# Performance work log

Measured on AMD Instinct MI355X. Metric: run time of the kernel, lower is better.

Reference implementation:

```python
import jax, jax.numpy as jnp
import numpy as np

B, S, E = 8, 1024, 1024
MS = 128            # modal_context seq len
NH = 16             # attention heads
NE = 8              # total experts (4 shared + 4 modality-specific)
TOP_K = 2
FF = 4 * E          # expert hidden dim
EPS = 1e-5


def layer_norm(x, w, b, eps=EPS):
    m = jnp.mean(x, axis=-1, keepdims=True)
    v = jnp.mean(jnp.square(x - m), axis=-1, keepdims=True)
    return (x - m) / jnp.sqrt(v + eps) * w + b


def mha(q_in, kv_in, in_w, in_b, out_w, out_b, nh=NH):
    # torch nn.MultiheadAttention (batch_first) equivalent, eval mode (no dropout)
    e = q_in.shape[-1]
    q = q_in @ in_w[:e].T + in_b[:e]
    k = kv_in @ in_w[e:2 * e].T + in_b[e:2 * e]
    v = kv_in @ in_w[2 * e:].T + in_b[2 * e:]
    b, sq, _ = q.shape
    sk = k.shape[1]
    hd = e // nh
    q = q.reshape(b, sq, nh, hd).transpose(0, 2, 1, 3)
    k = k.reshape(b, sk, nh, hd).transpose(0, 2, 1, 3)
    v = v.reshape(b, sk, nh, hd).transpose(0, 2, 1, 3)
    scores = jnp.einsum('bhqd,bhkd->bhqk', q, k) * (1.0 / np.sqrt(hd).astype(np.float32))
    attn = jax.nn.softmax(scores, axis=-1)
    o = jnp.einsum('bhqk,bhkd->bhqd', attn, v).transpose(0, 2, 1, 3).reshape(b, sq, e)
    return o @ out_w.T + out_b


def _forward(x, modal_context,
             attn_in_w, attn_in_b, attn_out_w, attn_out_b,
             xattn_in_w, xattn_in_b, xattn_out_w, xattn_out_b,
             norm1_w, norm1_b, norm2_w, norm2_b, norm3_w, norm3_b,
             xnorm_w, xnorm_b, router_w, router_b, gate_w, gate_b,
             exp_ln_w, exp_ln_b, exp_fc1_w, exp_fc1_b, exp_fc2_w, exp_fc2_b):
    # --- self-attention block (pre-norm residual) ---
    h = x + mha(layer_norm(x, norm1_w, norm1_b), layer_norm(x, norm1_w, norm1_b),
                attn_in_w, attn_in_b, attn_out_w, attn_out_b)
    # --- cross-modal fusion with sigmoid modal gate ---
    xn = layer_norm(h, xnorm_w, xnorm_b)
    fusion = mha(xn, modal_context, xattn_in_w, xattn_in_b, xattn_out_w, xattn_out_b)
    gate = jax.nn.sigmoid(xn @ gate_w.T + gate_b)
    h = h + gate * fusion
    # --- MoE block: AttentiveRouter (softmax + top-k renorm) over shared+modality experts ---
    xn2 = layer_norm(h, norm2_w, norm2_b)
    logits = xn2 @ router_w.T + router_b                  # [B,S,NE]
    probs = jax.nn.softmax(logits, axis=-1)
    topw, topi = jax.lax.top_k(probs, TOP_K)              # [B,S,K]
    topw = topw / jnp.sum(topw, axis=-1, keepdims=True)
    # scatter top-k weights to dense combine tensor [B,S,NE]
    combine = jnp.sum(jax.nn.one_hot(topi, NE, dtype=x.dtype) * topw[..., None], axis=-2)
    moe = jnp.zeros_like(h)
    for e_idx in range(NE):  # small fixed loop over experts
        xe = layer_norm(xn2, exp_ln_w[e_idx], exp_ln_b[e_idx])
        hh = jax.nn.gelu(xe @ exp_fc1_w[e_idx].T + exp_fc1_b[e_idx])
        oe = hh @ exp_fc2_w[e_idx].T + exp_fc2_b[e_idx]
        moe = moe + combine[..., e_idx:e_idx + 1] * oe
    out = h + moe
    return layer_norm(out, norm3_w, norm3_b)


def setup_inputs() -> dict:
    key = jax.random.key(0)
    ks = jax.random.split(key, 32)
    std = 0.02
    d = {
        'x': jax.random.normal(ks[0], (B, S, E), jnp.float32),
        'modal_context': jax.random.normal(ks[1], (B, MS, E), jnp.float32),
        'attn_in_w': jax.random.normal(ks[2], (3 * E, E), jnp.float32) * std,
        'attn_in_b': jnp.zeros((3 * E,), jnp.float32),
        'attn_out_w': jax.random.normal(ks[3], (E, E), jnp.float32) * std,
        'attn_out_b': jnp.zeros((E,), jnp.float32),
        'xattn_in_w': jax.random.normal(ks[4], (3 * E, E), jnp.float32) * std,
        'xattn_in_b': jnp.zeros((3 * E,), jnp.float32),
        'xattn_out_w': jax.random.normal(ks[5], (E, E), jnp.float32) * std,
        'xattn_out_b': jnp.zeros((E,), jnp.float32),
        'norm1_w': jnp.ones((E,), jnp.float32), 'norm1_b': jnp.zeros((E,), jnp.float32),
        'norm2_w': jnp.ones((E,), jnp.float32), 'norm2_b': jnp.zeros((E,), jnp.float32),
        'norm3_w': jnp.ones((E,), jnp.float32), 'norm3_b': jnp.zeros((E,), jnp.float32),
        'xnorm_w': jnp.ones((E,), jnp.float32), 'xnorm_b': jnp.zeros((E,), jnp.float32),
        'router_w': jax.random.normal(ks[6], (NE, E), jnp.float32) * 0.1 / np.sqrt(E).astype(np.float32),
        'router_b': jnp.zeros((NE,), jnp.float32),
        'gate_w': jax.random.normal(ks[7], (E, E), jnp.float32) * std,
        'gate_b': jnp.zeros((E,), jnp.float32),
        'exp_ln_w': jnp.ones((NE, E), jnp.float32),
        'exp_ln_b': jnp.zeros((NE, E), jnp.float32),
        'exp_fc1_w': jax.random.normal(ks[8], (NE, FF, E), jnp.float32) * std,
        'exp_fc1_b': jnp.zeros((NE, FF), jnp.float32),
        'exp_fc2_w': jax.random.normal(ks[9], (NE, E, FF), jnp.float32) * std,
        'exp_fc2_b': jnp.zeros((NE, E), jnp.float32),
    }
    return d


def reference(x, modal_context,
              attn_in_w, attn_in_b, attn_out_w, attn_out_b,
              xattn_in_w, xattn_in_b, xattn_out_w, xattn_out_b,
              norm1_w, norm1_b, norm2_w, norm2_b, norm3_w, norm3_b,
              xnorm_w, xnorm_b, router_w, router_b, gate_w, gate_b,
              exp_ln_w, exp_ln_b, exp_fc1_w, exp_fc1_b, exp_fc2_w, exp_fc2_b):
    return _forward(x, modal_context,
                    attn_in_w, attn_in_b, attn_out_w, attn_out_b,
                    xattn_in_w, xattn_in_b, xattn_out_w, xattn_out_b,
                    norm1_w, norm1_b, norm2_w, norm2_b, norm3_w, norm3_b,
                    xnorm_w, xnorm_b, router_w, router_b, gate_w, gate_b,
                    exp_ln_w, exp_ln_b, exp_fc1_w, exp_fc1_b, exp_fc2_w, exp_fc2_b)
```

## Files before the change

kernel.cpp:

```cpp
#include <hip/hip_runtime.h>
#include <cstdint>
#include <cstddef>
#include <math.h>

typedef unsigned short u16;
typedef __attribute__((ext_vector_type(4))) float f32x4;
typedef __attribute__((ext_vector_type(8))) short short8;
typedef __attribute__((ext_vector_type(4))) short short4v;

__device__ __forceinline__ float b2f(u16 u) {
    union { unsigned int i; float f; } v; v.i = ((unsigned int)u) << 16; return v.f;
}
__device__ __forceinline__ u16 f2b(float f) {
    union { float f; unsigned int i; } v; v.f = f;
    unsigned int i = v.i;
    return (u16)((i + 0x7FFFu + ((i >> 16) & 1u)) >> 16);
}
__device__ __forceinline__ void split3t(float a, short& h, short& m, short& l) {
    union { float f; unsigned int u; } va, vh, v1, vm, v2;
    va.f = a;
    vh.u = va.u & 0xFFFF0000u;
    float r1 = a - vh.f;
    v1.f = r1;
    vm.u = v1.u & 0xFFFF0000u;
    float r2 = r1 - vm.f;
    v2.f = r2;
    h = (short)(vh.u >> 16);
    m = (short)(vm.u >> 16);
    l = (short)(v2.u >> 16);
}
__device__ __forceinline__ float gelu_f(float x) {
    float x3 = x * x * x;
    float y = 0.7978845608028654f * (x + 0.044715f * x3);
    float ya = fminf(fabsf(y), 15.f);
    float e = expf(-2.f * ya);
    float t = (1.f - e) / (1.f + e);
    t = copysignf(t, y);
    return 0.5f * x * (1.f + t);
}

struct EGemmP {
    const float* A; int lda; long aSo, aSi; int aDiv;
    const float* B; int ldb; long bSo, bSi; int bDiv;
    float* C; int ldc; long cSo, cSi; int cDiv;
    const float* bias;
    const float* resid;
    const float* fus;
    int K;
};

template<int EPI, int WM, int WN, int MF, int NF>
__global__ __launch_bounds__(256)
void gemm_emu(EGemmP p)
{
    constexpr int TM = WM * MF * 16;
    constexpr int TN = WN * NF * 16;
    constexpr int TK = 32;
    __shared__ u16 Ah[TM * TK], Am[TM * TK], Al[TM * TK];
    __shared__ u16 Bh[TN * TK], Bm[TN * TK], Bl[TN * TK];
    const int tid = threadIdx.x;
    const int z = blockIdx.z;
    const float* Ab = p.A + (long)(z / p.aDiv) * p.aSo + (long)(z % p.aDiv) * p.aSi
                      + (long)blockIdx.x * TM * p.lda;
    const float* Bb = p.B + (long)(z / p.bDiv) * p.bSo + (long)(z % p.bDiv) * p.bSi
                      + (long)blockIdx.y * TN * p.ldb;
    const int lane = tid & 63;
    const int wv = tid >> 6;
    const int wm = wv / WN;
    const int wn = wv % WN;
    const int kg = lane >> 4;
    const int l16 = lane & 15;
    f32x4 acc[MF][NF];
#pragma unroll
    for (int m = 0; m < MF; ++m)
#pragma unroll
        for (int n = 0; n < NF; ++n)
            acc[m][n] = (f32x4){0.f, 0.f, 0.f, 0.f};

    for (int k0 = 0; k0 < p.K; k0 += TK) {
#pragma unroll
        for (int i = 0; i < (TM * TK) / 1024; ++i) {
            int e = i * 256 + tid;
            int r = e >> 3;
            int c = (e & 7) * 4;
            f32x4 a = *(const f32x4*)&Ab[(long)r * p.lda + k0 + c];
            short4v h, m, l;
#pragma unroll
            for (int j = 0; j < 4; ++j) {
                short th, tm2, tl2;
                split3t(a[j], th, tm2, tl2);
                h[j] = th; m[j] = tm2; l[j] = tl2;
            }
            *(short4v*)&Ah[r * TK + c] = h;
            *(short4v*)&Am[r * TK + c] = m;
            *(short4v*)&Al[r * TK + c] = l;
        }
#pragma unroll
        for (int i = 0; i < (TN * TK) / 1024; ++i) {
            int e = i * 256 + tid;
            int r = e >> 3;
            int c = (e & 7) * 4;
            f32x4 a = *(const f32x4*)&Bb[(long)r * p.ldb + k0 + c];
            short4v h, m, l;
#pragma unroll
            for (int j = 0; j < 4; ++j) {
                short th, tm2, tl2;
                split3t(a[j], th, tm2, tl2);
                h[j] = th; m[j] = tm2; l[j] = tl2;
            }
            *(short4v*)&Bh[r * TK + c] = h;
            *(short4v*)&Bm[r * TK + c] = m;
            *(short4v*)&Bl[r * TK + c] = l;
        }
        __syncthreads();
        short8 ah[MF], am[MF], al[MF], bh[NF], bm[NF], bl[NF];
#pragma unroll
        for (int m = 0; m < MF; ++m) {
            int ro = (wm * MF * 16 + m * 16 + l16) * TK + kg * 8;
            ah[m] = *(const short8*)&Ah[ro];
            am[m] = *(const short8*)&Am[ro];
            al[m] = *(const short8*)&Al[ro];
        }
#pragma unroll
        for (int n = 0; n < NF; ++n) {
            int ro = (wn * NF * 16 + n * 16 + l16) * TK + kg * 8;
            bh[n] = *(const short8*)&Bh[ro];
            bm[n] = *(const short8*)&Bm[ro];
            bl[n] = *(const short8*)&Bl[ro];
        }
#pragma unroll
        for (int m = 0; m < MF; ++m)
#pragma unroll
            for (int n = 0; n < NF; ++n) {
                f32x4 a = acc[m][n];
                a = __builtin_amdgcn_mfma_f32_16x16x32_bf16(al[m], bh[n], a, 0, 0, 0);
                a = __builtin_amdgcn_mfma_f32_16x16x32_bf16(ah[m], bl[n], a, 0, 0, 0);
                a = __builtin_amdgcn_mfma_f32_16x16x32_bf16(am[m], bm[n], a, 0, 0, 0);
                a = __builtin_amdgcn_mfma_f32_16x16x32_bf16(am[m], bh[n], a, 0, 0, 0);
                a = __builtin_amdgcn_mfma_f32_16x16x32_bf16(ah[m], bm[n], a, 0, 0, 0);
                a = __builtin_amdgcn_mfma_f32_16x16x32_bf16(ah[m], bh[n], a, 0, 0, 0);
                acc[m][n] = a;
            }
        __syncthreads();
    }
    const long cbase = (long)(z / p.cDiv) * p.cSo + (long)(z % p.cDiv) * p.cSi;
#pragma unroll
    for (int m = 0; m < MF; ++m)
#pragma unroll
        for (int n = 0; n < NF; ++n) {
            const int colt = blockIdx.y * TN + wn * NF * 16 + n * 16 + l16;
            float bv = p.bias ? p.bias[colt] : 0.f;
#pragma unroll
            for (int r = 0; r < 4; ++r) {
                const int rowt = blockIdx.x * TM + wm * MF * 16 + m * 16 + kg * 4 + r;
                const long idx = cbase + (long)rowt * p.ldc + colt;
                float v = acc[m][n][r] + bv;
                if constexpr (EPI == 0) {
                    p.C[idx] = v;
                } else if constexpr (EPI == 1) {
                    p.C[idx] = v + p.resid[idx];
                } else {
                    float g = 1.f / (1.f + expf(-v));
                    p.C[idx] = p.resid[idx] + g * p.fus[idx];
                }
            }
        }
}

struct MoeP {
    const u16* A; int lda;
    const u16* Bw; long bStrideE; int ldb;
    u16* HHo;
    float* M1; float* M2;
    int ldc;
    const float* biasE; long biasStride;
    const float* combine;
    const int* cnt;
    const int* pfx;
    const int* tlist;
    int K;
};

template<int EPI>
__global__ __launch_bounds__(256)
void gemm_moe(MoeP p)
{
    const int ex = blockIdx.z;
    const int count = p.cnt[ex];
    if ((int)(blockIdx.x * 128) >= count) return;
    const int base = p.pfx[ex];
    constexpr int TK = 32;
    __shared__ u16 lA[128 * TK];
    __shared__ u16 lB[128 * TK];
    const int tid = threadIdx.x;
    const u16* Ab = p.A + (long)(base + blockIdx.x * 128) * p.lda;
    const u16* Bb = p.Bw + (long)ex * p.bStrideE + (long)blockIdx.y * 128 * p.ldb;
    const int lane = tid & 63;
    const int wv = tid >> 6;
    const int wm = wv >> 1;
    const int wn = wv & 1;
    const int kg = lane >> 4;
    const int l16 = lane & 15;
    f32x4 acc[4][4];
#pragma unroll
    for (int m = 0; m < 4; ++m)
#pragma unroll
        for (int n = 0; n < 4; ++n)
            acc[m][n] = (f32x4){0.f, 0.f, 0.f, 0.f};

    for (int k0 = 0; k0 < p.K; k0 += TK) {
#pragma unroll
        for (int i = 0; i < 2; ++i) {
            int e = i * 256 + tid;
            int r = e >> 2;
            int c = (e & 3) * 8;
            *(short8*)&lA[r * TK + c] = *(const short8*)&Ab[(long)r * p.lda + k0 + c];
        }
#pragma unroll
        for (int i = 0; i < 2; ++i) {
            int e = i * 256 + tid;
            int r = e >> 2;
            int c = (e & 3) * 8;
            *(short8*)&lB[r * TK + c] = *(const short8*)&Bb[(long)r * p.ldb + k0 + c];
        }
        __syncthreads();
        short8 af[4], bfr[4];
#pragma unroll
        for (int m = 0; m < 4; ++m)
            af[m] = *(const short8*)&lA[(wm * 64 + m * 16 + l16) * TK + kg * 8];
#pragma unroll
        for (int n = 0; n < 4; ++n)
            bfr[n] = *(const short8*)&lB[(wn * 64 + n * 16 + l16) * TK + kg * 8];
#pragma unroll
        for (int m = 0; m < 4; ++m)
#pragma unroll
            for (int n = 0; n < 4; ++n)
                acc[m][n] = __builtin_amdgcn_mfma_f32_16x16x32_bf16(af[m], bfr[n], acc[m][n], 0, 0, 0);
        __syncthreads();
    }
    const float* bias = p.biasE + (long)ex * p.biasStride;
#pragma unroll
    for (int m = 0; m < 4; ++m)
#pragma unroll
        for (int n = 0; n < 4; ++n) {
            const int colt = blockIdx.y * 128 + wn * 64 + n * 16 + l16;
            const float bv = bias[colt];
#pragma unroll
            for (int r = 0; r < 4; ++r) {
                const int rowt = blockIdx.x * 128 + wm * 64 + m * 16 + kg * 4 + r;
                if (rowt >= count) continue;
                float v = acc[m][n][r] + bv;
                if constexpr (EPI == 3) {
                    p.HHo[(long)(base + rowt) * p.ldc + colt] = f2b(gelu_f(v));
                } else {
                    const int entry = p.tlist[ex * 8192 + rowt];
                    const int tok = entry & 0xFFFF;
                    const int k = entry >> 16;
                    const float w = p.combine[(long)tok * 8 + ex];
                    float* dst = k ? p.M2 : p.M1;
                    dst[(long)tok * p.ldc + colt] = w * v;
                }
            }
        }
}

template<int MODE>
__global__ __launch_bounds__(256)
void ln2p(const float* in, const float* add1, const float* add2,
          const float* w, const float* b, float* outf)
{
    const long row = blockIdx.x;
    const int t = threadIdx.x;
    const int c0 = t * 4;
    f32x4 v = *(const f32x4*)&in[row * 1024 + c0];
    if constexpr (MODE == 2) {
        f32x4 a1 = *(const f32x4*)&add1[row * 1024 + c0];
        f32x4 a2 = *(const f32x4*)&add2[row * 1024 + c0];
#pragma unroll
        for (int j = 0; j < 4; ++j) v[j] += a1[j] + a2[j];
    }
    __shared__ float r1[4], r2[4];
    const int lane = t & 63, wv = t >> 6;
    float s1 = v[0] + v[1] + v[2] + v[3];
    for (int o = 32; o; o >>= 1) s1 += __shfl_xor(s1, o);
    if (lane == 0) r1[wv] = s1;
    __syncthreads();
    const float mean = (r1[0] + r1[1] + r1[2] + r1[3]) * (1.f / 1024.f);
    f32x4 d;
#pragma unroll
    for (int j = 0; j < 4; ++j) d[j] = v[j] - mean;
    float s2 = d[0] * d[0] + d[1] * d[1] + d[2] * d[2] + d[3] * d[3];
    for (int o = 32; o; o >>= 1) s2 += __shfl_xor(s2, o);
    if (lane == 0) r2[wv] = s2;
    __syncthreads();
    const float var = (r2[0] + r2[1] + r2[2] + r2[3]) * (1.f / 1024.f);
    const float rstd = 1.f / sqrtf(var + 1e-5f);
    f32x4 o4;
#pragma unroll
    for (int j = 0; j < 4; ++j) o4[j] = d[j] * rstd * w[c0 + j] + b[c0 + j];
    *(f32x4*)&outf[row * 1024 + c0] = o4;
}

__global__ __launch_bounds__(256)
void rowstats(const float* in, float* st, int* cnt)
{
    if (blockIdx.x == 0 && threadIdx.x < 8) cnt[threadIdx.x] = 0;
    const long row = blockIdx.x;
    const int t = threadIdx.x;
    const int c0 = t * 4;
    f32x4 v = *(const f32x4*)&in[row * 1024 + c0];
    __shared__ float r1[4], r2[4];
    const int lane = t & 63, wv = t >> 6;
    float s1 = v[0] + v[1] + v[2] + v[3];
    for (int o = 32; o; o >>= 1) s1 += __shfl_xor(s1, o);
    if (lane == 0) r1[wv] = s1;
    __syncthreads();
    const float mean = (r1[0] + r1[1] + r1[2] + r1[3]) * (1.f / 1024.f);
    float s2 = 0.f;
#pragma unroll
    for (int j = 0; j < 4; ++j) { float d = v[j] - mean; s2 += d * d; }
    for (int o = 32; o; o >>= 1) s2 += __shfl_xor(s2, o);
    if (lane == 0) r2[wv] = s2;
    __syncthreads();
    if (t == 0) {
        const float var = (r2[0] + r2[1] + r2[2] + r2[3]) * (1.f / 1024.f);
        st[row * 2] = mean;
        st[row * 2 + 1] = 1.f / sqrtf(var + 1e-5f);
    }
}

__global__ __launch_bounds__(256)
void softmax_f32(float* sm, int C, float scale)
{
    const long row = blockIdx.x;
    float* p = sm + row * (long)C;
    const int t = threadIdx.x;
    const int idx = t * 4;
    const bool act = idx < C;
    f32x4 v = (f32x4){-1e30f, -1e30f, -1e30f, -1e30f};
    if (act) {
        v = *(const f32x4*)&p[idx];
#pragma unroll
        for (int j = 0; j < 4; ++j) v[j] *= scale;
    }
    float mx = fmaxf(fmaxf(v[0], v[1]), fmaxf(v[2], v[3]));
    for (int o = 32; o; o >>= 1) mx = fmaxf(mx, __shfl_xor(mx, o));
    __shared__ float red[4], red2[4];
    const int lane = t & 63, wv = t >> 6;
    if (lane == 0) red[wv] = mx;
    __syncthreads();
    mx = fmaxf(fmaxf(red[0], red[1]), fmaxf(red[2], red[3]));
    float e[4], s = 0.f;
    if (act) {
#pragma unroll
        for (int j = 0; j < 4; ++j) { e[j] = expf(v[j] - mx); s += e[j]; }
    }
    for (int o = 32; o; o >>= 1) s += __shfl_xor(s, o);
    if (lane == 0) red2[wv] = s;
    __syncthreads();
    s = red2[0] + red2[1] + red2[2] + red2[3];
    if (act) {
        f32x4 o4;
#pragma unroll
        for (int j = 0; j < 4; ++j) o4[j] = e[j] / s;
        *(f32x4*)&p[idx] = o4;
    }
}

__global__ __launch_bounds__(256)
void transpose64f(const float* src, int sld, long sSo, long sSi, int sDiv, float* dst, int Skv)
{
    const int z = blockIdx.y;
    const float* Sp = src + (long)(z / sDiv) * sSo + (long)(z % sDiv) * sSi;
    float* Dp = dst + (long)z * 64 * Skv;
    const int j0 = blockIdx.x * 64;
    __shared__ float tl[64][68];
    const int tid = threadIdx.x;
#pragma unroll
    for (int it = 0; it < 4; ++it) {
        int e = (it * 256 + tid) * 4;
        int r = e >> 6, c = e & 63;
        f32x4 d = *(const f32x4*)&Sp[(long)(j0 + r) * sld + c];
        *(f32x4*)&tl[r][c] = d;
    }
    __syncthreads();
    const int d0 = tid >> 2;
    const int jc = (tid & 3) * 16;
    float tmp[16];
#pragma unroll
    for (int i = 0; i < 16; ++i) tmp[i] = tl[jc + i][d0];
#pragma unroll
    for (int i = 0; i < 16; ++i) Dp[(long)d0 * Skv + j0 + jc + i] = tmp[i];
}

__global__ __launch_bounds__(256)
void router_k(const float* xn2, const float* rw, const float* rb, float* cmb,
              int* cnt, int* tlist)
{
    const int tok = blockIdx.x * 4 + (threadIdx.x >> 6);
    const int lane = threadIdx.x & 63;
    const float* xp = xn2 + (long)tok * 1024 + lane * 16;
    float xv[16];
#pragma unroll
    for (int j = 0; j < 16; ++j) xv[j] = xp[j];
    double acc[8];
#pragma unroll
    for (int e = 0; e < 8; ++e) {
        const float* wp = rw + e * 1024 + lane * 16;
        double s = 0.0;
#pragma unroll
        for (int j = 0; j < 16; ++j) s += (double)xv[j] * (double)wp[j];
        acc[e] = s;
    }
    for (int o = 32; o; o >>= 1) {
#pragma unroll
        for (int e = 0; e < 8; ++e) acc[e] += __shfl_xor(acc[e], o);
    }
    if (lane == 0) {
        double l[8];
#pragma unroll
        for (int e = 0; e < 8; ++e) l[e] = acc[e] + (double)rb[e];
        int i1 = 0;
#pragma unroll
        for (int e = 1; e < 8; ++e) if (l[e] > l[i1]) i1 = e;
        int i2 = (i1 == 0) ? 1 : 0;
#pragma unroll
        for (int e = 0; e < 8; ++e) if (e != i1 && l[e] > l[i2]) i2 = e;
        double w1 = 1.0 / (1.0 + exp(l[i2] - l[i1]));
        double w2 = 1.0 - w1;
        float c8[8] = {0, 0, 0, 0, 0, 0, 0, 0};
        c8[i1] = (float)w1;
        c8[i2] = (float)w2;
        float* cp = cmb + (long)tok * 8;
#pragma unroll
        for (int e = 0; e < 8; ++e) cp[e] = c8[e];
        int s1 = atomicAdd(&cnt[i1], 1);
        tlist[i1 * 8192 + s1] = tok;
        int s2 = atomicAdd(&cnt[i2], 1);
        tlist[i2 * 8192 + s2] = tok | 65536;
    }
}

__global__ void prefix8(const int* cnt, int* pfx)
{
    if (threadIdx.x == 0) {
        int s = 0;
#pragma unroll
        for (int e = 0; e < 8; ++e) { pfx[e] = s; s += cnt[e]; }
    }
}

__global__ __launch_bounds__(256)
void gather_all(const float* xn2, const float* st, const int* cnt, const int* pfx,
                const int* tlist, const float* lnw, const float* lnb, u16* xe)
{
    const int e = blockIdx.y;
    const int slot = blockIdx.x;
    if (slot >= cnt[e]) return;
    const int tok = tlist[e * 8192 + slot] & 0xFFFF;
    const int c0 = threadIdx.x * 4;
    f32x4 v = *(const f32x4*)&xn2[(long)tok * 1024 + c0];
    const float m = st[tok * 2], r = st[tok * 2 + 1];
    const float* w = lnw + (long)e * 1024;
    const float* b = lnb + (long)e * 1024;
    short4v o4;
#pragma unroll
    for (int j = 0; j < 4; ++j) o4[j] = (short)f2b((v[j] - m) * r * w[c0 + j] + b[c0 + j]);
    *(short4v*)&xe[(long)(pfx[e] + slot) * 1024 + c0] = o4;
}

__global__ __launch_bounds__(256)
void cvtw(const float* in, u16* out, long n4)
{
    const long stride = (long)gridDim.x * 256;
    for (long i = (long)blockIdx.x * 256 + threadIdx.x; i < n4; i += stride) {
        f32x4 v = *(const f32x4*)&in[i * 4];
        short4v o;
#pragma unroll
        for (int j = 0; j < 4; ++j) o[j] = (short)f2b(v[j]);
        *(short4v*)&out[i * 4] = o;
    }
}

extern "C" void kernel_launch(void* const* d_in, const int* in_sizes, int n_in,
                              void* d_out, int out_size, void* d_ws, size_t ws_size,
                              hipStream_t stream)
{
    (void)in_sizes; (void)n_in; (void)out_size;
    const float* x          = (const float*)d_in[0];
    const float* modal      = (const float*)d_in[1];
    const float* attn_in_w  = (const float*)d_in[2];
    const float* attn_in_b  = (const float*)d_in[3];
    const float* attn_out_w = (const float*)d_in[4];
    const float* attn_out_b = (const float*)d_in[5];
    const float* xattn_in_w = (const float*)d_in[6];
    const float* xattn_in_b = (const float*)d_in[7];
    const float* xattn_out_w= (const float*)d_in[8];
    const float* xattn_out_b= (const float*)d_in[9];
    const float* norm1_w = (const float*)d_in[10];
    const float* norm1_b = (const float*)d_in[11];
    const float* norm2_w = (const float*)d_in[12];
    const float* norm2_b = (const float*)d_in[13];
    const float* norm3_w = (const float*)d_in[14];
    const float* norm3_b = (const float*)d_in[15];
    const float* xnorm_w = (const float*)d_in[16];
    const float* xnorm_b = (const float*)d_in[17];
    const float* router_w = (const float*)d_in[18];
    const float* router_b = (const float*)d_in[19];
    const float* gate_w = (const float*)d_in[20];
    const float* gate_b = (const float*)d_in[21];
    const float* exp_ln_w = (const float*)d_in[22];
    const float* exp_ln_b = (const float*)d_in[23];
    const float* exp_fc1_w = (const float*)d_in[24];
    const float* exp_fc1_b = (const float*)d_in[25];
    const float* exp_fc2_w = (const float*)d_in[26];
    const float* exp_fc2_b = (const float*)d_in[27];

    char* wsb = (char*)d_ws;
    size_t off = 0;
    auto AL = [&](size_t bytes) { size_t r = off; off += (bytes + 255) & ~(size_t)255; return r; };
    float* XN  = (float*)(wsb + AL(33554432));
    float* H   = (float*)(wsb + AL(33554432));
    float* H2  = (float*)(wsb + AL(33554432));
    float* XN2 = (float*)(wsb + AL(33554432));
    float* FUS = (float*)(wsb + AL(33554432));
    float* MOE = (float*)(wsb + AL(33554432));
    float* XKV = (float*)(wsb + AL(8388608));
    float* CMB = (float*)(wsb + AL(262144));
    float* ST  = (float*)(wsb + AL(65536));
    int*   CNT = (int*)(wsb + AL(256));
    int*   PFX = (int*)(wsb + AL(256));
    int*   TLS = (int*)(wsb + AL(262144));
    char*  RA  = wsb + AL(100663296);
    char*  RB  = wsb + AL(100663296);
    if (off > ws_size) return;

    float* QKV = (float*)RA;
    float* XQ  = (float*)RA;
    float* XO  = (float*)(RA + 33554432);
    float* SCf = (float*)RB;
    float* VTf = (float*)(RB + 67108864);
    u16*   HH  = (u16*)RA;
    u16*   XE  = (u16*)(RA + 135266304);
    u16*   WB  = (u16*)XN;
    float* out = (float*)d_out;

    ln2p<0><<<8192, 256, 0, stream>>>(x, nullptr, nullptr, norm1_w, norm1_b, XN);

    {
        EGemmP p{XN, 1024, 0, 0, 1, attn_in_w, 1024, 0, 0, 1,
                 QKV, 3072, 0, 0, 1, attn_in_b, nullptr, nullptr, 1024};
        gemm_emu<0, 2, 2, 4, 2><<<dim3(64, 48, 1), 256, 0, stream>>>(p);
    }
    transpose64f<<<dim3(16, 128), 256, 0, stream>>>(QKV + 2048, 3072, (long)1024 * 3072, 64, 16, VTf, 1024);

    for (int g = 0; g < 8; ++g) {
        EGemmP s{QKV + (long)g * 1024 * 3072, 3072, 0, 64, 16,
                 QKV + 1024 + (long)g * 1024 * 3072, 3072, 0, 64, 16,
                 SCf, 1024, 0, (long)1024 * 1024, 16, nullptr, nullptr, nullptr, 64};
        gemm_emu<0, 2, 2, 4, 2><<<dim3(8, 16, 16), 256, 0, stream>>>(s);

        softmax_f32<<<16 * 1024, 256, 0, stream>>>(SCf, 1024, 0.125f);

        EGemmP v{SCf, 1024, 0, (long)1024 * 1024, 16,
                 VTf + (long)g * 16 * 64 * 1024, 1024, 0, (long)64 * 1024, 16,
                 XN + (long)g * 1024 * 1024, 1024, 0, 64, 16, nullptr, nullptr, nullptr, 1024};
        gemm_emu<0, 2, 2, 2, 2><<<dim3(16, 1, 16), 256, 0, stream>>>(v);
    }

    {
        EGemmP p{XN, 1024, 0, 0, 1, attn_out_w, 1024, 0, 0, 1,
                 H, 1024, 0, 0, 1, attn_out_b, x, nullptr, 1024};
        gemm_emu<1, 2, 2, 4, 2><<<dim3(64, 16, 1), 256, 0, stream>>>(p);
    }
    ln2p<0><<<8192, 256, 0, stream>>>(H, nullptr, nullptr, xnorm_w, xnorm_b, XN);

    {
        EGemmP p{XN, 1024, 0, 0, 1, xattn_in_w, 1024, 0, 0, 1,
                 XQ, 1024, 0, 0, 1, xattn_in_b, nullptr, nullptr, 1024};
        gemm_emu<0, 2, 2, 4, 2><<<dim3(64, 16, 1), 256, 0, stream>>>(p);
    }
    {
        EGemmP p{modal, 1024, 0, 0, 1, xattn_in_w + (size_t)1024 * 1024, 1024, 0, 0, 1,
                 XKV, 2048, 0, 0, 1, xattn_in_b + 1024, nullptr, nullptr, 1024};
        gemm_emu<0, 2, 2, 4, 2><<<dim3(8, 32, 1), 256, 0, stream>>>(p);
    }
    transpose64f<<<dim3(2, 128), 256, 0, stream>>>(XKV + 1024, 2048, (long)128 * 2048, 64, 16, VTf, 128);

    {
        EGemmP s{XQ, 1024, (long)1024 * 1024, 64, 16,
                 XKV, 2048, (long)128 * 2048, 64, 16,
                 SCf, 128, 0, (long)1024 * 128, 1 << 20, nullptr, nullptr, nullptr, 64};
        gemm_emu<0, 2, 2, 4, 2><<<dim3(8, 2, 128), 256, 0, stream>>>(s);
    }
    softmax_f32<<<128 * 1024, 256, 0, stream>>>(SCf, 128, 0.125f);
    {
        EGemmP v{SCf, 128, 0, (long)1024 * 128, 1 << 20,
                 VTf, 128, 0, (long)64 * 128, 1 << 20,
                 XO, 1024, (long)1024 * 1024, 64, 16, nullptr, nullptr, nullptr, 128};
        gemm_emu<0, 2, 2, 4, 2><<<dim3(8, 1, 128), 256, 0, stream>>>(v);
    }
    {
        EGemmP p{XO, 1024, 0, 0, 1, xattn_out_w, 1024, 0, 0, 1,
                 FUS, 1024, 0, 0, 1, xattn_out_b, nullptr, nullptr, 1024};
        gemm_emu<0, 2, 2, 4, 2><<<dim3(64, 16, 1), 256, 0, stream>>>(p);
    }
    {
        EGemmP p{XN, 1024, 0, 0, 1, gate_w, 1024, 0, 0, 1,
                 H2, 1024, 0, 0, 1, gate_b, H, FUS, 1024};
        gemm_emu<2, 2, 2, 4, 2><<<dim3(64, 16, 1), 256, 0, stream>>>(p);
    }
    ln2p<0><<<8192, 256, 0, stream>>>(H2, nullptr, nullptr, norm2_w, norm2_b, XN2);
    rowstats<<<8192, 256, 0, stream>>>(XN2, ST, CNT);
    router_k<<<2048, 256, 0, stream>>>(XN2, router_w, router_b, CMB, CNT, TLS);
    prefix8<<<1, 64, 0, stream>>>(CNT, PFX);

    gather_all<<<dim3(8192, 8), 256, 0, stream>>>(XN2, ST, CNT, PFX, TLS, exp_ln_w, exp_ln_b, XE);
    cvtw<<<2048, 256, 0, stream>>>(exp_fc1_w, WB, 8388608);
    {
        MoeP p1{XE, 1024, WB, (long)4096 * 1024, 1024,
                HH, nullptr, nullptr, 4096,
                exp_fc1_b, 4096, nullptr, CNT, PFX, TLS, 1024};
        gemm_moe<3><<<dim3(64, 32, 8), 256, 0, stream>>>(p1);
    }
    cvtw<<<2048, 256, 0, stream>>>(exp_fc2_w, WB, 8388608);
    {
        MoeP p2{HH, 4096, WB, (long)1024 * 4096, 4096,
                nullptr, MOE, FUS, 1024,
                exp_fc2_b, 1024, CMB, CNT, PFX, TLS, 4096};
        gemm_moe<4><<<dim3(64, 8, 8), 256, 0, stream>>>(p2);
    }

    ln2p<2><<<8192, 256, 0, stream>>>(H2, MOE, FUS, norm3_w, norm3_b, out);
}
```

Measured before the change: 2.996 ms.

## Use direct global-to-LDS loads with XOR swizzle and larger K tile in MoE GEMM

The MoE expert GEMM now loads A and B tiles straight from global memory into LDS with global_load_lds 16-byte transfers, skipping the trip through registers. The K tile doubles from 32 to 64, and an XOR swizzle on the 8-element column groups cuts LDS bank conflicts when fragments are read for MFMA. This means fewer barriers per K and less VGPR pressure, at the cost of twice the LDS per block and reliance on the direct-to-LDS load path.

```diff
diff --git a/kernel.cpp b/kernel.cpp
--- a/kernel.cpp
+++ b/kernel.cpp
@@ -37,6 +37,13 @@
     float t = (1.f - e) / (1.f + e);
     t = copysignf(t, y);
     return 0.5f * x * (1.f + t);
+}
+__device__ __forceinline__ void gld16(const u16* g, u16* l)
+{
+    __builtin_amdgcn_global_load_lds(
+        (const __attribute__((address_space(1))) void*)(g),
+        (__attribute__((address_space(3))) void*)(l),
+        16, 0, 0);
 }
 
 struct EGemmP {
@@ -189,9 +196,9 @@
     const int count = p.cnt[ex];
     if ((int)(blockIdx.x * 128) >= count) return;
     const int base = p.pfx[ex];
-    constexpr int TK = 32;
-    __shared__ u16 lA[128 * TK];
-    __shared__ u16 lB[128 * TK];
+    constexpr int TK = 64;
+    __shared__ __align__(16) u16 lA[128 * TK];
+    __shared__ __align__(16) u16 lB[128 * TK];
     const int tid = threadIdx.x;
     const u16* Ab = p.A + (long)(base + blockIdx.x * 128) * p.lda;
     const u16* Bb = p.Bw + (long)ex * p.bStrideE + (long)blockIdx.y * 128 * p.ldb;
@@ -210,32 +217,35 @@
 
     for (int k0 = 0; k0 < p.K; k0 += TK) {
 #pragma unroll
-        for (int i = 0; i < 2; ++i) {
+        for (int i = 0; i < 4; ++i) {
             int e = i * 256 + tid;
-            int r = e >> 2;
-            int c = (e & 3) * 8;
-            *(short8*)&lA[r * TK + c] = *(const short8*)&Ab[(long)r * p.lda + k0 + c];
-        }
-#pragma unroll
-        for (int i = 0; i < 2; ++i) {
-            int e = i * 256 + tid;
-            int r = e >> 2;
-            int c = (e & 3) * 8;
-            *(short8*)&lB[r * TK + c] = *(const short8*)&Bb[(long)r * p.ldb + k0 + c];
+            int r = e >> 3;
+            int jg = (e & 7) ^ (r & 7);
+            gld16(&Ab[(long)r * p.lda + k0 + jg * 8], &lA[e * 8]);
+            gld16(&Bb[(long)r * p.ldb + k0 + jg * 8], &lB[e * 8]);
         }
         __syncthreads();
-        short8 af[4], bfr[4];
-#pragma unroll
-        for (int m = 0; m < 4; ++m)
-            af[m] = *(const short8*)&lA[(wm * 64 + m * 16 + l16) * TK + kg * 8];
-#pragma unroll
-        for (int n = 0; n < 4; ++n)
-            bfr[n] = *(const short8*)&lB[(wn * 64 + n * 16 + l16) * TK + kg * 8];
-#pragma unroll
-        for (int m = 0; m < 4; ++m)
-#pragma unroll
-            for (int n = 0; n < 4; ++n)
-                acc[m][n] = __builtin_amdgcn_mfma_f32_16x16x32_bf16(af[m], bfr[n], acc[m][n], 0, 0, 0);
+#pragma unroll
+        for (int ks = 0; ks < 2; ++ks) {
+            short8 af[4], bfr[4];
+#pragma unroll
+            for (int m = 0; m < 4; ++m) {
+                int row = wm * 64 + m * 16 + l16;
+                int jj = (ks * 4 + kg) ^ (row & 7);
+                af[m] = *(const short8*)&lA[row * TK + jj * 8];
+            }
+#pragma unroll
+            for (int n = 0; n < 4; ++n) {
+                int row = wn * 64 + n * 16 + l16;
+                int jj = (ks * 4 + kg) ^ (row & 7);
+                bfr[n] = *(const short8*)&lB[row * TK + jj * 8];
+            }
+#pragma unroll
+            for (int m = 0; m < 4; ++m)
+#pragma unroll
+                for (int n = 0; n < 4; ++n)
+                    acc[m][n] = __builtin_amdgcn_mfma_f32_16x16x32_bf16(af[m], bfr[n], acc[m][n], 0, 0, 0);
+        }
         __syncthreads();
     }
     const float* bias = p.biasE + (long)ex * p.biasStride;
```

Measured after the change: 2.853 ms. 4.8% less time.
